# Optimization experiments

Measured on AMD Instinct MI355X. Metric: run time of the kernel, lower is better.

## Reference

```python
import jax, jax.numpy as jnp
import numpy as np


def setup_inputs() -> dict:
    key = jax.random.key(0)
    k1, k2 = jax.random.split(key)
    N = 8192
    similarity = jax.random.normal(k1, (N, N), dtype=jnp.float32)
    text_to_img_mapping = jax.random.randint(k2, (N,), 0, N, dtype=jnp.int64)
    return {"similarity": similarity, "text_to_img_mapping": text_to_img_mapping}


def reference(similarity, text_to_img_mapping):
    n_text, n_img = similarity.shape
    rows = jnp.arange(n_text)
    # text->image CE: mean over text rows of -log_softmax(sim, axis=1)[i, map[i]]
    lsm_rows = jax.nn.log_softmax(similarity, axis=1)
    text_loss = -jnp.mean(lsm_rows[rows, text_to_img_mapping])
    # image->text CE with multi-hot soft targets mask[img, txt] = 1 iff map[txt] == img.
    # -sum(mask * log_softmax(sim.T, axis=1)) / n_img
    #   == -sum_i log_softmax(sim, axis=0)[i, map[i]] / n_img  (gather, no NxN mask)
    lsm_cols = jax.nn.log_softmax(similarity, axis=0)
    visual_loss = -jnp.sum(lsm_cols[rows, text_to_img_mapping]) / n_img
    return (text_loss + visual_loss) / 2.0
```

## Files before the change

kernel.cpp:

```cpp
#include <hip/hip_runtime.h>
#include <hip/hip_bf16.h>
#include <math.h>

#define N 8192
#define RB 32
#define T1 512
#define CPT (N / T1)
#define NRC (N / RB)


__global__ __launch_bounds__(T1)
void stage1(const float* __restrict__ sim,
            float* __restrict__ colS,
            float* __restrict__ rowLSE) {
    const int tid = threadIdx.x;
    const int rc = blockIdx.x;
    const int rowBase = rc * RB;
    const int wave = tid >> 6, lane = tid & 63;

    float cs[CPT];
    #pragma unroll
    for (int k = 0; k < CPT; ++k) cs[k] = 0.f;

    __shared__ float lsum[RB][8];

    for (int r = 0; r < RB; ++r) {
        const float4* p = (const float4*)(sim + (size_t)(rowBase + r) * N);
        float4 v[CPT / 4];
        #pragma unroll
        for (int k = 0; k < CPT / 4; ++k)
            v[k] = p[tid + k * T1];

        float rs = 0.f;
        #pragma unroll
        for (int k = 0; k < CPT / 4; ++k) {
            float e0 = __expf(v[k].x), e1 = __expf(v[k].y);
            float e2 = __expf(v[k].z), e3 = __expf(v[k].w);
            cs[4 * k + 0] += e0; cs[4 * k + 1] += e1;
            cs[4 * k + 2] += e2; cs[4 * k + 3] += e3;
            rs += (e0 + e1) + (e2 + e3);
        }
        #pragma unroll
        for (int off = 32; off >= 1; off >>= 1)
            rs += __shfl_xor(rs, off);
        if (lane == 0) lsum[r][wave] = rs;
    }
    __syncthreads();

    if (tid < RB) {
        float s = 0.f;
        #pragma unroll
        for (int w = 0; w < 8; ++w) s += lsum[tid][w];
        rowLSE[rowBase + tid] = __logf(s);
    }

    float4* outp = (float4*)(colS + (size_t)rc * N);
    #pragma unroll
    for (int k = 0; k < CPT / 4; ++k)
        outp[tid + k * T1] = make_float4(cs[4 * k + 0], cs[4 * k + 1],
                                         cs[4 * k + 2], cs[4 * k + 3]);
}

__global__ __launch_bounds__(64)
void stage2(const float* __restrict__ colS, float* __restrict__ colLSE) {
    const int g = blockIdx.x * 64 + threadIdx.x;
    float s = 0.f;
    #pragma unroll 8
    for (int rc = 0; rc < NRC; ++rc)
        s += colS[(size_t)rc * N + g];
    colLSE[g] = __logf(s);
}

__global__ __launch_bounds__(256)
void stage3(const float* __restrict__ sim, const long long* __restrict__ map,
            const float* __restrict__ rowLSE, const float* __restrict__ colLSE,
            float* __restrict__ partial) {
    const int i = blockIdx.x * 256 + threadIdx.x;
    const int c = (int)map[i];
    float val = rowLSE[i] + colLSE[c] - 2.0f * sim[(size_t)i * N + c];
    #pragma unroll
    for (int off = 32; off >= 1; off >>= 1)
        val += __shfl_xor(val, off);
    __shared__ float red[4];
    const int wave = threadIdx.x >> 6, lane = threadIdx.x & 63;
    if (lane == 0) red[wave] = val;
    __syncthreads();
    if (threadIdx.x == 0)
        partial[blockIdx.x] = red[0] + red[1] + red[2] + red[3];
}

__global__ __launch_bounds__(64)
void stage4(const float* __restrict__ partial, float* __restrict__ out) {
    float v = (threadIdx.x < 32) ? partial[threadIdx.x] : 0.f;
    #pragma unroll
    for (int off = 32; off >= 1; off >>= 1)
        v += __shfl_xor(v, off);
    if (threadIdx.x == 0)
        out[0] = v / (2.0f * (float)N);
}

extern "C" void kernel_launch(void* const* d_in, const int* in_sizes, int n_in,
                              void* d_out, int out_size, void* d_ws, size_t ws_size,
                              hipStream_t stream) {
    const float* sim = (const float*)d_in[0];
    const long long* map = (const long long*)d_in[1];
    float* out = (float*)d_out;

    float* ws = (float*)d_ws;
    float* colS   = ws;
    float* rowLSE = colS + (size_t)NRC * N;
    float* colLSE = rowLSE + N;
    float* partial = colLSE + N;

    stage1<<<NRC, T1, 0, stream>>>(sim, colS, rowLSE);
    stage2<<<N / 64, 64, 0, stream>>>(colS, colLSE);
    stage3<<<N / 256, 256, 0, stream>>>(sim, map, rowLSE, colLSE, partial);
    stage4<<<1, 64, 0, stream>>>(partial, out);
}
```

Before: 60.73 us.

## Tile stage1 over a 2D row/column grid and merge row-sum reduction into stage2

The exp-sum pass now tiles the matrix into 64-row by 2048-column blocks on a 2D grid instead of giving each block 32 full rows. Each block writes partial row sums per column chunk, and stage2 folds those chunks into the row log-sum-exp alongside the column reduction. Doubling the row tile halves the column-partials buffer that stage1 writes and stage2 reads, and smaller blocks may schedule more flexibly. In exchange stage2 runs with far fewer blocks (32), which reduces parallelism in that reduction, and there is an extra small row-partials buffer.

```diff
diff --git a/kernel.cpp b/kernel.cpp
--- a/kernel.cpp
+++ b/kernel.cpp
@@ -3,67 +3,74 @@
 #include <math.h>
 
 #define N 8192
-#define RB 32
-#define T1 512
-#define CPT (N / T1)
+#define RB 64
+#define CB 2048
+#define T1 256
 #define NRC (N / RB)
+#define NCC (N / CB)
 
 
 __global__ __launch_bounds__(T1)
 void stage1(const float* __restrict__ sim,
             float* __restrict__ colS,
-            float* __restrict__ rowLSE) {
+            float* __restrict__ rowS) {
     const int tid = threadIdx.x;
-    const int rc = blockIdx.x;
+    const int cc = blockIdx.x;
+    const int rc = blockIdx.y;
+    const int colBase = cc * CB;
     const int rowBase = rc * RB;
-    const int wave = tid >> 6, lane = tid & 63;
 
-    float cs[CPT];
+    float cs[8];
     #pragma unroll
-    for (int k = 0; k < CPT; ++k) cs[k] = 0.f;
+    for (int k = 0; k < 8; ++k) cs[k] = 0.f;
 
-    __shared__ float lsum[RB][8];
+    __shared__ float lrow[RB][T1 / 4 + 1];
 
+    #pragma unroll 2
     for (int r = 0; r < RB; ++r) {
-        const float4* p = (const float4*)(sim + (size_t)(rowBase + r) * N);
-        float4 v[CPT / 4];
-        #pragma unroll
-        for (int k = 0; k < CPT / 4; ++k)
-            v[k] = p[tid + k * T1];
+        const float4* p = (const float4*)(sim + (size_t)(rowBase + r) * N + colBase);
+        float4 v0 = p[tid];
+        float4 v1 = p[tid + T1];
 
-        float rs = 0.f;
-        #pragma unroll
-        for (int k = 0; k < CPT / 4; ++k) {
-            float e0 = __expf(v[k].x), e1 = __expf(v[k].y);
-            float e2 = __expf(v[k].z), e3 = __expf(v[k].w);
-            cs[4 * k + 0] += e0; cs[4 * k + 1] += e1;
-            cs[4 * k + 2] += e2; cs[4 * k + 3] += e3;
-            rs += (e0 + e1) + (e2 + e3);
-        }
-        #pragma unroll
-        for (int off = 32; off >= 1; off >>= 1)
-            rs += __shfl_xor(rs, off);
-        if (lane == 0) lsum[r][wave] = rs;
+        float e0 = __expf(v0.x), e1 = __expf(v0.y), e2 = __expf(v0.z), e3 = __expf(v0.w);
+        float e4 = __expf(v1.x), e5 = __expf(v1.y), e6 = __expf(v1.z), e7 = __expf(v1.w);
+        cs[0] += e0; cs[1] += e1; cs[2] += e2; cs[3] += e3;
+        cs[4] += e4; cs[5] += e5; cs[6] += e6; cs[7] += e7;
+
+        float rp = ((e0 + e1) + (e2 + e3)) + ((e4 + e5) + (e6 + e7));
+        rp += __shfl_xor(rp, 1);
+        rp += __shfl_xor(rp, 2);
+        if ((tid & 3) == 0) lrow[r][tid >> 2] = rp;
     }
     __syncthreads();
 
-    if (tid < RB) {
+    {
+        const int r = tid >> 2, j = tid & 3;
         float s = 0.f;
         #pragma unroll
-        for (int w = 0; w < 8; ++w) s += lsum[tid][w];
-        rowLSE[rowBase + tid] = __logf(s);
+        for (int k = 0; k < (T1 / 4) / 4; ++k)
+            s += lrow[r][j + 4 * k];
+        s += __shfl_xor(s, 1);
+        s += __shfl_xor(s, 2);
+        if (j == 0) rowS[(size_t)cc * N + rowBase + r] = s;
     }
 
-    float4* outp = (float4*)(colS + (size_t)rc * N);
-    #pragma unroll
-    for (int k = 0; k < CPT / 4; ++k)
-        outp[tid + k * T1] = make_float4(cs[4 * k + 0], cs[4 * k + 1],
-                                         cs[4 * k + 2], cs[4 * k + 3]);
+    float4* outp = (float4*)(colS + (size_t)rc * N + colBase);
+    outp[tid]      = make_float4(cs[0], cs[1], cs[2], cs[3]);
+    outp[tid + T1] = make_float4(cs[4], cs[5], cs[6], cs[7]);
 }
 
-__global__ __launch_bounds__(64)
-void stage2(const float* __restrict__ colS, float* __restrict__ colLSE) {
-    const int g = blockIdx.x * 64 + threadIdx.x;
+__global__ __launch_bounds__(256)
+void stage2(const float* __restrict__ colS, const float* __restrict__ rowS,
+            float* __restrict__ colLSE, float* __restrict__ rowLSE) {
+    const int g = blockIdx.x * 256 + threadIdx.x;
+
+    float rs = 0.f;
+    #pragma unroll
+    for (int cc = 0; cc < NCC; ++cc)
+        rs += rowS[(size_t)cc * N + g];
+    rowLSE[g] = __logf(rs);
+
     float s = 0.f;
     #pragma unroll 8
     for (int rc = 0; rc < NRC; ++rc)
@@ -107,13 +114,15 @@
     float* out = (float*)d_out;
 
     float* ws = (float*)d_ws;
-    float* colS   = ws;
-    float* rowLSE = colS + (size_t)NRC * N;
-    float* colLSE = rowLSE + N;
+    float* colS    = ws;
+    float* rowS    = colS + (size_t)NRC * N;
+    float* rowLSE  = rowS + (size_t)NCC * N;
+    float* colLSE  = rowLSE + N;
     float* partial = colLSE + N;
 
-    stage1<<<NRC, T1, 0, stream>>>(sim, colS, rowLSE);
-    stage2<<<N / 64, 64, 0, stream>>>(colS, colLSE);
+    dim3 g1(NCC, NRC);
+    stage1<<<g1, T1, 0, stream>>>(sim, colS, rowS);
+    stage2<<<N / 256, 256, 0, stream>>>(colS, rowS, colLSE, rowLSE);
     stage3<<<N / 256, 256, 0, stream>>>(sim, map, rowLSE, colLSE, partial);
     stage4<<<1, 64, 0, stream>>>(partial, out);
 }
```

New measurement: 65.62 us. +8.1%, slower.

## Fuse row LSE and gather into stage1, split column reduction across slices

Applied to the files above, without the earlier changes.

Stage1 now gathers the target logit per row and reduces the row log-sum-exps into a per-block partial. It writes row sums to shared memory instead of doing per-row wave shuffles. Stage2 spreads each column's 256-entry reduction over 8 waves per block for more memory parallelism. Stage3 and stage4 merge into one single-block kernel that gathers colLSE through the mapping, which drops one launch. The serialized single-thread gather inside the row loop and the 64KB of shared memory per block may cost stage1 some latency and occupancy.

```diff
diff --git a/kernel.cpp b/kernel.cpp
--- a/kernel.cpp
+++ b/kernel.cpp
@@ -5,98 +5,133 @@
 #define N 8192
 #define RB 32
 #define T1 512
-#define CPT (N / T1)
 #define NRC (N / RB)
+#define CPT 16
 
 
 __global__ __launch_bounds__(T1)
-void stage1(const float* __restrict__ sim,
+void stage1(const float* __restrict__ sim, const long long* __restrict__ map,
             float* __restrict__ colS,
-            float* __restrict__ rowLSE) {
+            float* __restrict__ blkPart) {
     const int tid = threadIdx.x;
     const int rc = blockIdx.x;
     const int rowBase = rc * RB;
-    const int wave = tid >> 6, lane = tid & 63;
 
     float cs[CPT];
     #pragma unroll
     for (int k = 0; k < CPT; ++k) cs[k] = 0.f;
 
-    __shared__ float lsum[RB][8];
+    __shared__ float lrow[RB][T1];
+    __shared__ float rowLog[RB];
 
+    float gsum = 0.f;
+
+    #pragma unroll 2
     for (int r = 0; r < RB; ++r) {
-        const float4* p = (const float4*)(sim + (size_t)(rowBase + r) * N);
-        float4 v[CPT / 4];
-        #pragma unroll
-        for (int k = 0; k < CPT / 4; ++k)
-            v[k] = p[tid + k * T1];
+        const int row = rowBase + r;
+        const float4* p = (const float4*)(sim + (size_t)row * N);
+        float4 v0 = p[tid];
+        float4 v1 = p[tid + T1];
+        float4 v2 = p[tid + 2 * T1];
+        float4 v3 = p[tid + 3 * T1];
 
-        float rs = 0.f;
-        #pragma unroll
-        for (int k = 0; k < CPT / 4; ++k) {
-            float e0 = __expf(v[k].x), e1 = __expf(v[k].y);
-            float e2 = __expf(v[k].z), e3 = __expf(v[k].w);
-            cs[4 * k + 0] += e0; cs[4 * k + 1] += e1;
-            cs[4 * k + 2] += e2; cs[4 * k + 3] += e3;
-            rs += (e0 + e1) + (e2 + e3);
+        if (tid == 0) {
+            int c = (int)map[row];
+            gsum += sim[(size_t)row * N + c];
         }
-        #pragma unroll
-        for (int off = 32; off >= 1; off >>= 1)
-            rs += __shfl_xor(rs, off);
-        if (lane == 0) lsum[r][wave] = rs;
+
+        float e0 = __expf(v0.x), e1 = __expf(v0.y), e2 = __expf(v0.z), e3 = __expf(v0.w);
+        float e4 = __expf(v1.x), e5 = __expf(v1.y), e6 = __expf(v1.z), e7 = __expf(v1.w);
+        float e8 = __expf(v2.x), e9 = __expf(v2.y), eA = __expf(v2.z), eB = __expf(v2.w);
+        float eC = __expf(v3.x), eD = __expf(v3.y), eE = __expf(v3.z), eF = __expf(v3.w);
+
+        cs[0] += e0; cs[1] += e1; cs[2]  += e2; cs[3]  += e3;
+        cs[4] += e4; cs[5] += e5; cs[6]  += e6; cs[7]  += e7;
+        cs[8] += e8; cs[9] += e9; cs[10] += eA; cs[11] += eB;
+        cs[12] += eC; cs[13] += eD; cs[14] += eE; cs[15] += eF;
+
+        float rp = (((e0 + e1) + (e2 + e3)) + ((e4 + e5) + (e6 + e7)))
+                 + (((e8 + e9) + (eA + eB)) + ((eC + eD) + (eE + eF)));
+        lrow[r][tid] = rp;
     }
     __syncthreads();
 
-    if (tid < RB) {
+    {
+        const int r = tid >> 4, j = tid & 15;
         float s = 0.f;
         #pragma unroll
-        for (int w = 0; w < 8; ++w) s += lsum[tid][w];
-        rowLSE[rowBase + tid] = __logf(s);
+        for (int k = 0; k < T1 / 16; ++k)
+            s += lrow[r][j + 16 * k];
+        s += __shfl_xor(s, 1);
+        s += __shfl_xor(s, 2);
+        s += __shfl_xor(s, 4);
+        s += __shfl_xor(s, 8);
+        if (j == 0) rowLog[r] = __logf(s);
+    }
+    __syncthreads();
+
+    if (tid == 0) {
+        float b = -2.0f * gsum;
+        #pragma unroll
+        for (int r = 0; r < RB; ++r) b += rowLog[r];
+        blkPart[rc] = b;
     }
 
     float4* outp = (float4*)(colS + (size_t)rc * N);
-    #pragma unroll
-    for (int k = 0; k < CPT / 4; ++k)
-        outp[tid + k * T1] = make_float4(cs[4 * k + 0], cs[4 * k + 1],
-                                         cs[4 * k + 2], cs[4 * k + 3]);
+    outp[tid]          = make_float4(cs[0],  cs[1],  cs[2],  cs[3]);
+    outp[tid + T1]     = make_float4(cs[4],  cs[5],  cs[6],  cs[7]);
+    outp[tid + 2 * T1] = make_float4(cs[8],  cs[9],  cs[10], cs[11]);
+    outp[tid + 3 * T1] = make_float4(cs[12], cs[13], cs[14], cs[15]);
 }
 
-__global__ __launch_bounds__(64)
+__global__ __launch_bounds__(512)
 void stage2(const float* __restrict__ colS, float* __restrict__ colLSE) {
-    const int g = blockIdx.x * 64 + threadIdx.x;
+    const int tid = threadIdx.x;
+    const int cl = tid & 63;
+    const int slice = tid >> 6;
+    const int g = blockIdx.x * 64 + cl;
+
     float s = 0.f;
-    #pragma unroll 8
-    for (int rc = 0; rc < NRC; ++rc)
-        s += colS[(size_t)rc * N + g];
-    colLSE[g] = __logf(s);
+    #pragma unroll 4
+    for (int k = 0; k < NRC / 8; ++k)
+        s += colS[(size_t)(slice * (NRC / 8) + k) * N + g];
+
+    __shared__ float lds[8][64];
+    lds[slice][cl] = s;
+    __syncthreads();
+
+    if (tid < 64) {
+        float t = 0.f;
+        #pragma unroll
+        for (int w = 0; w < 8; ++w) t += lds[w][tid];
+        colLSE[blockIdx.x * 64 + tid] = __logf(t);
+    }
 }
 
-__global__ __launch_bounds__(256)
-void stage3(const float* __restrict__ sim, const long long* __restrict__ map,
-            const float* __restrict__ rowLSE, const float* __restrict__ colLSE,
-            float* __restrict__ partial) {
-    const int i = blockIdx.x * 256 + threadIdx.x;
-    const int c = (int)map[i];
-    float val = rowLSE[i] + colLSE[c] - 2.0f * sim[(size_t)i * N + c];
+__global__ __launch_bounds__(1024)
+void stage3(const long long* __restrict__ map,
+            const float* __restrict__ colLSE, const float* __restrict__ blkPart,
+            float* __restrict__ out) {
+    const int tid = threadIdx.x;
+    float v = (tid < NRC) ? blkPart[tid] : 0.f;
     #pragma unroll
-    for (int off = 32; off >= 1; off >>= 1)
-        val += __shfl_xor(val, off);
-    __shared__ float red[4];
-    const int wave = threadIdx.x >> 6, lane = threadIdx.x & 63;
-    if (lane == 0) red[wave] = val;
-    __syncthreads();
-    if (threadIdx.x == 0)
-        partial[blockIdx.x] = red[0] + red[1] + red[2] + red[3];
-}
-
-__global__ __launch_bounds__(64)
-void stage4(const float* __restrict__ partial, float* __restrict__ out) {
-    float v = (threadIdx.x < 32) ? partial[threadIdx.x] : 0.f;
+    for (int k = 0; k < N / 1024; ++k) {
+        int i = k * 1024 + tid;
+        v += colLSE[(int)map[i]];
+    }
     #pragma unroll
     for (int off = 32; off >= 1; off >>= 1)
         v += __shfl_xor(v, off);
-    if (threadIdx.x == 0)
-        out[0] = v / (2.0f * (float)N);
+    __shared__ float red[16];
+    const int wave = tid >> 6, lane = tid & 63;
+    if (lane == 0) red[wave] = v;
+    __syncthreads();
+    if (tid == 0) {
+        float t = 0.f;
+        #pragma unroll
+        for (int w = 0; w < 16; ++w) t += red[w];
+        out[0] = t / (2.0f * (float)N);
+    }
 }
 
 extern "C" void kernel_launch(void* const* d_in, const int* in_sizes, int n_in,
@@ -107,13 +142,11 @@
     float* out = (float*)d_out;
 
     float* ws = (float*)d_ws;
-    float* colS   = ws;
-    float* rowLSE = colS + (size_t)NRC * N;
-    float* colLSE = rowLSE + N;
-    float* partial = colLSE + N;
+    float* colS    = ws;
+    float* colLSE  = colS + (size_t)NRC * N;
+    float* blkPart = colLSE + N;
 
-    stage1<<<NRC, T1, 0, stream>>>(sim, colS, rowLSE);
-    stage2<<<N / 64, 64, 0, stream>>>(colS, colLSE);
-    stage3<<<N / 256, 256, 0, stream>>>(sim, map, rowLSE, colLSE, partial);
-    stage4<<<1, 64, 0, stream>>>(partial, out);
+    stage1<<<NRC, T1, 0, stream>>>(sim, map, colS, blkPart);
+    stage2<<<N / 64, 512, 0, stream>>>(colS, colLSE);
+    stage3<<<1, 1024, 0, stream>>>(map, colLSE, blkPart, out);
 }
```

Result: faster. 56.02 us (-7.7%).
